# Optimization experiments

Hardware: AMD Instinct MI355X
Metric: run time of the kernel (lower is better)

The kernel has to match this reference:

```python
import jax, jax.numpy as jnp
import numpy as np

N_NODES = 50000
N_EDGES = 600000
IN_DIM = 64
HID = 128
LN_EPS = 1e-5


def setup_inputs() -> dict:
    key = jax.random.key(0)
    ks = jax.random.split(key, 10)
    x = jax.random.normal(ks[0], (N_NODES, IN_DIM), dtype=jnp.float32)
    edge_index = jax.random.randint(ks[1], (2, N_EDGES), 0, N_NODES, dtype=jnp.int64)
    def lin(k, fan_in, fan_out):
        bound = 1.0 / np.sqrt(fan_in)
        kw, kb = jax.random.split(k)
        W = jax.random.uniform(kw, (fan_in, fan_out), minval=-bound, maxval=bound, dtype=jnp.float32)
        b = jax.random.uniform(kb, (fan_out,), minval=-bound, maxval=bound, dtype=jnp.float32)
        return W, b
    W1, b1 = lin(ks[2], IN_DIM, HID)
    W2, b2 = lin(ks[3], HID, HID)
    W3, b3 = lin(ks[4], HID, HID)
    g1 = jnp.ones((HID,), jnp.float32); be1 = jnp.zeros((HID,), jnp.float32)
    g2 = jnp.ones((HID,), jnp.float32); be2 = jnp.zeros((HID,), jnp.float32)
    g3 = jnp.ones((HID,), jnp.float32); be3 = jnp.zeros((HID,), jnp.float32)
    return dict(x=x, edge_index=edge_index, W1=W1, b1=b1, W2=W2, b2=b2, W3=W3, b3=b3,
                g1=g1, be1=be1, g2=g2, be2=be2, g3=g3, be3=be3)


def _gnn_layer(h, W, b, src, dst, inv_cnt, g, be):
    # linear transform then mean aggregation over {neighbors ∪ self} (self-loops in src/dst)
    h = h @ W + b                                   # [N, HID]
    s = jax.ops.segment_sum(h[src], dst, num_segments=N_NODES)  # gather + scatter-sum
    h = s * inv_cnt                                 # mean aggregation
    h = jax.nn.relu(h)
    mu = jnp.mean(h, axis=-1, keepdims=True)
    var = jnp.var(h, axis=-1, keepdims=True)
    return g * (h - mu) * jax.lax.rsqrt(var + LN_EPS) + be


def reference(x, edge_index, W1, b1, W2, b2, W3, b3, g1, be1, g2, be2, g3, be3):
    loops = jnp.arange(N_NODES, dtype=edge_index.dtype)
    src = jnp.concatenate([edge_index[0], loops])   # message source (x_j)
    dst = jnp.concatenate([edge_index[1], loops])   # aggregation target
    cnt = jax.ops.segment_sum(jnp.ones_like(dst, dtype=x.dtype), dst, num_segments=N_NODES)
    inv_cnt = (1.0 / cnt)[:, None]                  # cnt >= 1 due to self loops
    h = _gnn_layer(x, W1, b1, src, dst, inv_cnt, g1, be1)
    h = _gnn_layer(h, W2, b2, src, dst, inv_cnt, g2, be2)
    h = _gnn_layer(h, W3, b3, src, dst, inv_cnt, g3, be3)
    return h
```

## Files before the change

kernel.cpp:

```cpp
#include <hip/hip_runtime.h>
#include <hip/hip_bf16.h>

#define N_NODES 50000
#define N_EDGES 600000
#define HID 128
#define LN_EPS 1e-5f

#define SCAN_BLOCK 1024
#define SCAN_NBLK ((N_NODES + SCAN_BLOCK - 1) / SCAN_BLOCK)

typedef __attribute__((ext_vector_type(8))) short bf16x8;
typedef __attribute__((ext_vector_type(4))) float f32x4;

static __device__ __forceinline__ unsigned short f2bf(float f) {
    union { float f; unsigned u; } v; v.f = f;
    unsigned u = v.u;
    u += 0x7fffu + ((u >> 16) & 1u);
    return (unsigned short)(u >> 16);
}
static __device__ __forceinline__ float bflo(unsigned u) {
    union { unsigned u; float f; } c; c.u = u << 16; return c.f;
}
static __device__ __forceinline__ float bfhi(unsigned u) {
    union { unsigned u; float f; } c; c.u = u & 0xffff0000u; return c.f;
}

__global__ __launch_bounds__(256) void count_kernel(const int* __restrict__ ei,
                                                    int* __restrict__ deg, int E) {
    int i = blockIdx.x * blockDim.x + threadIdx.x;
    if (i < E) atomicAdd(&deg[ei[E + i]], 1);
}

__global__ __launch_bounds__(SCAN_BLOCK) void deg_partial_kernel(const int* __restrict__ deg,
                                                                 int* __restrict__ partials, int n) {
    int t = threadIdx.x;
    int i = blockIdx.x * SCAN_BLOCK + t;
    int v = (i < n) ? deg[i] : 0;
    int s = v;
#pragma unroll
    for (int off = 1; off < 64; off <<= 1) s += __shfl_xor(s, off);
    __shared__ int ws[SCAN_BLOCK / 64];
    if ((t & 63) == 0) ws[t >> 6] = s;
    __syncthreads();
    if (t == 0) {
        int tot = 0;
#pragma unroll
        for (int w = 0; w < SCAN_BLOCK / 64; ++w) tot += ws[w];
        partials[blockIdx.x] = tot;
    }
}

__global__ __launch_bounds__(64) void scan_partials_kernel(int* __restrict__ partials,
                                                           int* __restrict__ row_ptr, int nblk) {
    int lane = threadIdx.x;
    int v = (lane < nblk) ? partials[lane] : 0;
    int incl = v;
#pragma unroll
    for (int off = 1; off < 64; off <<= 1) {
        int x = __shfl_up(incl, off);
        if (lane >= off) incl += x;
    }
    if (lane < nblk) partials[lane] = incl - v;
    if (lane == 63) row_ptr[N_NODES] = incl;
}

__global__ __launch_bounds__(SCAN_BLOCK) void scan_final_kernel(const int* __restrict__ deg,
                                                                const int* __restrict__ partials,
                                                                int* __restrict__ row_ptr,
                                                                int* __restrict__ cursor,
                                                                float* __restrict__ inv_cnt, int n) {
    int t = threadIdx.x;
    int i = blockIdx.x * SCAN_BLOCK + t;
    int v = (i < n) ? deg[i] : 0;
    int lane = t & 63, wid = t >> 6;
    int incl = v;
#pragma unroll
    for (int off = 1; off < 64; off <<= 1) {
        int x = __shfl_up(incl, off);
        if (lane >= off) incl += x;
    }
    __shared__ int ws[SCAN_BLOCK / 64];
    if (lane == 63) ws[wid] = incl;
    __syncthreads();
    int woff = 0;
    for (int w = 0; w < wid; ++w) woff += ws[w];
    int excl = partials[blockIdx.x] + woff + (incl - v);
    if (i < n) {
        row_ptr[i] = excl;
        cursor[i]  = excl;
        inv_cnt[i] = 1.0f / (float)(v + 1);
    }
}

__global__ __launch_bounds__(256) void fill_kernel(const int* __restrict__ ei,
                                                   int* __restrict__ cursor,
                                                   int* __restrict__ col, int E) {
    int i = blockIdx.x * blockDim.x + threadIdx.x;
    if (i < E) {
        int s = ei[i];
        int d = ei[E + i];
        int p = atomicAdd(&cursor[d], 1);
        col[p] = s;
    }
}

__global__ __launch_bounds__(256) void wswz_all_kernel(const float* __restrict__ W1,
                                                       const float* __restrict__ W2,
                                                       const float* __restrict__ W3,
                                                       unsigned short* __restrict__ d1,
                                                       unsigned short* __restrict__ d2,
                                                       unsigned short* __restrict__ d3) {
    int i = blockIdx.x * 256 + threadIdx.x;
    const float* W; unsigned short* dst; int idx;
    if (i < 64 * 128)              { W = W1; dst = d1; idx = i; }
    else if (i < (64 + 128) * 128) { W = W2; dst = d2; idx = i - 64 * 128; }
    else if (i < (64 + 256) * 128) { W = W3; dst = d3; idx = i - (64 + 128) * 128; }
    else return;
    int k = idx >> 7, col = idx & 127;
    dst[(((k >> 3) * 128) + col) * 8 + (k & 7)] = f2bf(W[idx]);
}

template <int K, int AF32>
__global__ __launch_bounds__(256) void gemm_mfma_kernel(
    const void* __restrict__ Ap,
    const unsigned short* __restrict__ Wswz,
    const float* __restrict__ bias,
    unsigned short* __restrict__ out, int N) {
    __shared__ unsigned short Bl[K * 128];
    __shared__ float bl[128];
    int t = threadIdx.x;
    for (int i = t; i < K * 16; i += 256)
        ((int4*)Bl)[i] = ((const int4*)Wswz)[i];
    if (t < 128) bl[t] = bias[t];
    __syncthreads();

    int lane = t & 63;
    int w = t >> 6;
    int r0 = blockIdx.x * 64 + w * 16;
    int colb = lane & 15;
    int kg = lane >> 4;
    int rowa = min(r0 + colb, N - 1);

    f32x4 acc[8];
#pragma unroll
    for (int c = 0; c < 8; ++c) acc[c] = (f32x4){0.f, 0.f, 0.f, 0.f};

    const bf16x8* Blv = (const bf16x8*)Bl;
    for (int s = 0; s < K; s += 32) {
        bf16x8 afrag;
        if (AF32) {
            const float* Af = (const float*)Ap;
            float4 a0 = *(const float4*)&Af[(size_t)rowa * K + s + kg * 8];
            float4 a1 = *(const float4*)&Af[(size_t)rowa * K + s + kg * 8 + 4];
            afrag[0] = (short)f2bf(a0.x); afrag[1] = (short)f2bf(a0.y);
            afrag[2] = (short)f2bf(a0.z); afrag[3] = (short)f2bf(a0.w);
            afrag[4] = (short)f2bf(a1.x); afrag[5] = (short)f2bf(a1.y);
            afrag[6] = (short)f2bf(a1.z); afrag[7] = (short)f2bf(a1.w);
        } else {
            const unsigned short* Ab = (const unsigned short*)Ap;
            afrag = *(const bf16x8*)&Ab[(size_t)rowa * K + s + kg * 8];
        }
        int kb = (s >> 3) + kg;
#pragma unroll
        for (int c = 0; c < 8; ++c) {
            bf16x8 bfrag = Blv[kb * 128 + c * 16 + colb];
            acc[c] = __builtin_amdgcn_mfma_f32_16x16x32_bf16(afrag, bfrag, acc[c], 0, 0, 0);
        }
    }
#pragma unroll
    for (int c = 0; c < 8; ++c) {
        int col = c * 16 + colb;
        float bv = bl[col];
#pragma unroll
        for (int r = 0; r < 4; ++r) {
            int ro = r0 + kg * 4 + r;
            if (ro < N) out[(size_t)ro * 128 + col] = f2bf(acc[c][r] + bv);
        }
    }
}

template <int BF16OUT>
__global__ __launch_bounds__(256) void agg_norm_kernel(
    const unsigned short* __restrict__ hb,
    const int* __restrict__ row_ptr,
    const int* __restrict__ col,
    const float* __restrict__ inv_cnt,
    const float* __restrict__ g, const float* __restrict__ be,
    void* __restrict__ outp, int N) {
    int tid  = blockIdx.x * 256 + threadIdx.x;
    int wave = tid >> 6;
    int lane = threadIdx.x & 63;
    int sub  = lane >> 4;
    int lc   = lane & 15;
    int n    = wave * 4 + sub;
    bool act = n < N;
    int nc   = act ? n : N - 1;

    const uint4* h4 = (const uint4*)hb;

    float a[8];
    {
        uint4 u = h4[(size_t)nc * 16 + lc];
        a[0] = bflo(u.x); a[1] = bfhi(u.x);
        a[2] = bflo(u.y); a[3] = bfhi(u.y);
        a[4] = bflo(u.z); a[5] = bfhi(u.z);
        a[6] = bflo(u.w); a[7] = bfhi(u.w);
    }

    int beg = row_ptr[nc], end = row_ptr[nc + 1];
    int cnt = end - beg;
    int lim = min(cnt, 32);
    int c0 = (lc < cnt)      ? col[beg + lc]      : nc;
    int c1 = (16 + lc < cnt) ? col[beg + 16 + lc] : nc;

    int wlim = lim;
    wlim = max(wlim, __shfl_xor(wlim, 16));
    wlim = max(wlim, __shfl_xor(wlim, 32));
    int nGrp = (wlim + 7) >> 3;

    for (int gi = 0; gi < nGrp; ++gi) {
        int e0 = gi * 8;
        int jj[8]; float mm[8];
#pragma unroll
        for (int q = 0; q < 8; ++q) {
            int iq = max(min(e0 + q, lim - 1), 0);
            mm[q] = (e0 + q < lim) ? 1.0f : 0.0f;
            int sl = sub * 16 + (iq & 15);
            int jA = __shfl(c0, sl);
            int jB = __shfl(c1, sl);
            jj[q] = (iq < 16) ? jA : jB;
        }
        uint4 u[8];
#pragma unroll
        for (int q = 0; q < 8; ++q) u[q] = h4[(size_t)jj[q] * 16 + lc];
#pragma unroll
        for (int q = 0; q < 8; ++q) {
            a[0] = fmaf(mm[q], bflo(u[q].x), a[0]); a[1] = fmaf(mm[q], bfhi(u[q].x), a[1]);
            a[2] = fmaf(mm[q], bflo(u[q].y), a[2]); a[3] = fmaf(mm[q], bfhi(u[q].y), a[3]);
            a[4] = fmaf(mm[q], bflo(u[q].z), a[4]); a[5] = fmaf(mm[q], bfhi(u[q].z), a[5]);
            a[6] = fmaf(mm[q], bflo(u[q].w), a[6]); a[7] = fmaf(mm[q], bfhi(u[q].w), a[7]);
        }
    }
    for (int e = 32; e < cnt; ++e) {
        int j = col[beg + e];
        uint4 u = h4[(size_t)j * 16 + lc];
        a[0] += bflo(u.x); a[1] += bfhi(u.x);
        a[2] += bflo(u.y); a[3] += bfhi(u.y);
        a[4] += bflo(u.z); a[5] += bfhi(u.z);
        a[6] += bflo(u.w); a[7] += bfhi(u.w);
    }

    float ic = inv_cnt[nc];
    float s[8], sum = 0.f, sq = 0.f;
#pragma unroll
    for (int k = 0; k < 8; ++k) {
        s[k] = fmaxf(a[k] * ic, 0.0f);
        sum += s[k];
        sq  += s[k] * s[k];
    }
#pragma unroll
    for (int off = 1; off < 16; off <<= 1) {
        sum += __shfl_xor(sum, off);
        sq  += __shfl_xor(sq, off);
    }
    float mu  = sum * (1.0f / 128.0f);
    float var = sq * (1.0f / 128.0f) - mu * mu;
    float rs  = rsqrtf(var + LN_EPS);

    const float4* gv  = (const float4*)g;
    const float4* bv  = (const float4*)be;
    float4 gA = gv[lc * 2], gB = gv[lc * 2 + 1];
    float4 bA = bv[lc * 2], bB = bv[lc * 2 + 1];
    float o[8];
    o[0] = gA.x * (s[0] - mu) * rs + bA.x;
    o[1] = gA.y * (s[1] - mu) * rs + bA.y;
    o[2] = gA.z * (s[2] - mu) * rs + bA.z;
    o[3] = gA.w * (s[3] - mu) * rs + bA.w;
    o[4] = gB.x * (s[4] - mu) * rs + bB.x;
    o[5] = gB.y * (s[5] - mu) * rs + bB.y;
    o[6] = gB.z * (s[6] - mu) * rs + bB.z;
    o[7] = gB.w * (s[7] - mu) * rs + bB.w;

    if (!act) return;
    if (BF16OUT) {
        uint4 p;
        p.x = (unsigned)f2bf(o[0]) | ((unsigned)f2bf(o[1]) << 16);
        p.y = (unsigned)f2bf(o[2]) | ((unsigned)f2bf(o[3]) << 16);
        p.z = (unsigned)f2bf(o[4]) | ((unsigned)f2bf(o[5]) << 16);
        p.w = (unsigned)f2bf(o[6]) | ((unsigned)f2bf(o[7]) << 16);
        ((uint4*)outp)[(size_t)nc * 16 + lc] = p;
    } else {
        float4 f0; f0.x = o[0]; f0.y = o[1]; f0.z = o[2]; f0.w = o[3];
        float4 f1; f1.x = o[4]; f1.y = o[5]; f1.z = o[6]; f1.w = o[7];
        ((float4*)outp)[(size_t)nc * 32 + lc * 2]     = f0;
        ((float4*)outp)[(size_t)nc * 32 + lc * 2 + 1] = f1;
    }
}

extern "C" void kernel_launch(void* const* d_in, const int* in_sizes, int n_in,
                              void* d_out, int out_size, void* d_ws, size_t ws_size,
                              hipStream_t stream) {
    const float* x  = (const float*)d_in[0];
    const int*   ei = (const int*)d_in[1];
    const float* W1 = (const float*)d_in[2];
    const float* b1 = (const float*)d_in[3];
    const float* W2 = (const float*)d_in[4];
    const float* b2 = (const float*)d_in[5];
    const float* W3 = (const float*)d_in[6];
    const float* b3 = (const float*)d_in[7];
    const float* g1 = (const float*)d_in[8];
    const float* be1 = (const float*)d_in[9];
    const float* g2 = (const float*)d_in[10];
    const float* be2 = (const float*)d_in[11];
    const float* g3 = (const float*)d_in[12];
    const float* be3 = (const float*)d_in[13];
    float* out = (float*)d_out;

    const int N = N_NODES, E = N_EDGES;
    char* w = (char*)d_ws;
    unsigned short* hb   = (unsigned short*)w; w += (size_t)N * 128 * 2;
    unsigned short* midb = (unsigned short*)w; w += (size_t)N * 128 * 2;
    unsigned short* w1s  = (unsigned short*)w; w += (size_t)64 * 128 * 2;
    unsigned short* w2s  = (unsigned short*)w; w += (size_t)128 * 128 * 2;
    unsigned short* w3s  = (unsigned short*)w; w += (size_t)128 * 128 * 2;
    int*   col    = (int*)w;    w += (size_t)E * sizeof(int);
    int*   rowp   = (int*)w;    w += (size_t)(N + 1) * sizeof(int);
    int*   cursor = (int*)w;    w += (size_t)N * sizeof(int);
    int*   deg    = (int*)w;    w += (size_t)N * sizeof(int);
    float* invc   = (float*)w;  w += (size_t)N * sizeof(float);
    int*   parts  = (int*)w;    w += (size_t)SCAN_NBLK * sizeof(int);

    hipMemsetAsync(deg, 0, (size_t)N * sizeof(int), stream);
    count_kernel<<<(E + 255) / 256, 256, 0, stream>>>(ei, deg, E);
    deg_partial_kernel<<<SCAN_NBLK, SCAN_BLOCK, 0, stream>>>(deg, parts, N);
    scan_partials_kernel<<<1, 64, 0, stream>>>(parts, rowp, SCAN_NBLK);
    scan_final_kernel<<<SCAN_NBLK, SCAN_BLOCK, 0, stream>>>(deg, parts, rowp, cursor, invc, N);
    fill_kernel<<<(E + 255) / 256, 256, 0, stream>>>(ei, cursor, col, E);

    wswz_all_kernel<<<((64 + 256) * 128 + 255) / 256, 256, 0, stream>>>(W1, W2, W3, w1s, w2s, w3s);

    const int gemm_blocks = (N + 63) / 64;
    const int agg_blocks  = (N + 15) / 16;

    gemm_mfma_kernel<64, 1><<<gemm_blocks, 256, 0, stream>>>(x, w1s, b1, hb, N);
    agg_norm_kernel<1><<<agg_blocks, 256, 0, stream>>>(hb, rowp, col, invc, g1, be1, midb, N);
    gemm_mfma_kernel<128, 0><<<gemm_blocks, 256, 0, stream>>>(midb, w2s, b2, hb, N);
    agg_norm_kernel<1><<<agg_blocks, 256, 0, stream>>>(hb, rowp, col, invc, g2, be2, midb, N);
    gemm_mfma_kernel<128, 0><<<gemm_blocks, 256, 0, stream>>>(midb, w3s, b3, hb, N);
    agg_norm_kernel<0><<<agg_blocks, 256, 0, stream>>>(hb, rowp, col, invc, g3, be3, out, N);
}
```

Measured before the change: 196.7 us.

## Fuse layer-1 GEMM, degree count, and weight swizzle into one launch; drop scan-partials kernel

Merges the first-layer GEMM (which now swizzles W1 into shared memory itself), the degree-counting atomics and the weight swizzle into one heterogeneous kernel whose blocks are split by block index. It also removes the single-block partials scan: each block of the final scan now sums the preceding partials serially in thread 0. The goal is fewer kernel launches and letting independent work run concurrently. In exchange, every GEMM block re-converts W1 and thread 0 does a serial loop over about 49 partials per block.

```diff
diff --git a/kernel.cpp b/kernel.cpp
--- a/kernel.cpp
+++ b/kernel.cpp
@@ -8,6 +8,10 @@
 
 #define SCAN_BLOCK 1024
 #define SCAN_NBLK ((N_NODES + SCAN_BLOCK - 1) / SCAN_BLOCK)
+
+#define GB1 ((N_NODES + 63) / 64)
+#define CB  ((N_EDGES + 255) / 256)
+#define WB  (((64 + 256) * 128) / 256)
 
 typedef __attribute__((ext_vector_type(8))) short bf16x8;
 typedef __attribute__((ext_vector_type(4))) float f32x4;
@@ -25,10 +29,82 @@
     union { unsigned u; float f; } c; c.u = u & 0xffff0000u; return c.f;
 }
 
-__global__ __launch_bounds__(256) void count_kernel(const int* __restrict__ ei,
-                                                    int* __restrict__ deg, int E) {
-    int i = blockIdx.x * blockDim.x + threadIdx.x;
-    if (i < E) atomicAdd(&deg[ei[E + i]], 1);
+__global__ __launch_bounds__(256) void mega1_kernel(
+    const float* __restrict__ x,
+    const unsigned short* __restrict__ W1swz,
+    const float* __restrict__ b1,
+    unsigned short* __restrict__ hb,
+    const int* __restrict__ ei,
+    int* __restrict__ deg,
+    const float* __restrict__ W1,
+    const float* __restrict__ W2,
+    const float* __restrict__ W3,
+    unsigned short* __restrict__ d1,
+    unsigned short* __restrict__ d2,
+    unsigned short* __restrict__ d3, int N, int E) {
+    __shared__ unsigned short Bl[64 * 128];
+    __shared__ float bl[128];
+    int bid = blockIdx.x;
+    int t = threadIdx.x;
+
+    if (bid < GB1) {
+        for (int i = t; i < 64 * 128; i += 256) {
+            int k = i >> 7, col = i & 127;
+            Bl[(((k >> 3) * 128) + col) * 8 + (k & 7)] = f2bf(W1[i]);
+        }
+        if (t < 128) bl[t] = b1[t];
+        __syncthreads();
+
+        int lane = t & 63;
+        int w = t >> 6;
+        int r0 = bid * 64 + w * 16;
+        int colb = lane & 15;
+        int kg = lane >> 4;
+        int rowa = min(r0 + colb, N - 1);
+
+        f32x4 acc[8];
+#pragma unroll
+        for (int c = 0; c < 8; ++c) acc[c] = (f32x4){0.f, 0.f, 0.f, 0.f};
+
+        const bf16x8* Blv = (const bf16x8*)Bl;
+        for (int s = 0; s < 64; s += 32) {
+            bf16x8 afrag;
+            float4 a0 = *(const float4*)&x[(size_t)rowa * 64 + s + kg * 8];
+            float4 a1 = *(const float4*)&x[(size_t)rowa * 64 + s + kg * 8 + 4];
+            afrag[0] = (short)f2bf(a0.x); afrag[1] = (short)f2bf(a0.y);
+            afrag[2] = (short)f2bf(a0.z); afrag[3] = (short)f2bf(a0.w);
+            afrag[4] = (short)f2bf(a1.x); afrag[5] = (short)f2bf(a1.y);
+            afrag[6] = (short)f2bf(a1.z); afrag[7] = (short)f2bf(a1.w);
+            int kb = (s >> 3) + kg;
+#pragma unroll
+            for (int c = 0; c < 8; ++c) {
+                bf16x8 bfrag = Blv[kb * 128 + c * 16 + colb];
+                acc[c] = __builtin_amdgcn_mfma_f32_16x16x32_bf16(afrag, bfrag, acc[c], 0, 0, 0);
+            }
+        }
+#pragma unroll
+        for (int c = 0; c < 8; ++c) {
+            int col = c * 16 + colb;
+            float bv = bl[col];
+#pragma unroll
+            for (int r = 0; r < 4; ++r) {
+                int ro = r0 + kg * 4 + r;
+                if (ro < N) hb[(size_t)ro * 128 + col] = f2bf(acc[c][r] + bv);
+            }
+        }
+    } else if (bid < GB1 + CB) {
+        int i = (bid - GB1) * 256 + t;
+        if (i < E) atomicAdd(&deg[ei[E + i]], 1);
+    } else {
+        int i = (bid - GB1 - CB) * 256 + t;
+        const float* W; unsigned short* dst; int idx;
+        if (i < 64 * 128)              { W = W1; dst = d1; idx = i; }
+        else if (i < (64 + 128) * 128) { W = W2; dst = d2; idx = i - 64 * 128; }
+        else if (i < (64 + 256) * 128) { W = W3; dst = d3; idx = i - (64 + 128) * 128; }
+        else return;
+        int k = idx >> 7, col = idx & 127;
+        dst[(((k >> 3) * 128) + col) * 8 + (k & 7)] = f2bf(W[idx]);
+    }
 }
 
 __global__ __launch_bounds__(SCAN_BLOCK) void deg_partial_kernel(const int* __restrict__ deg,
@@ -50,26 +126,24 @@
     }
 }
 
-__global__ __launch_bounds__(64) void scan_partials_kernel(int* __restrict__ partials,
-                                                           int* __restrict__ row_ptr, int nblk) {
-    int lane = threadIdx.x;
-    int v = (lane < nblk) ? partials[lane] : 0;
-    int incl = v;
-#pragma unroll
-    for (int off = 1; off < 64; off <<= 1) {
-        int x = __shfl_up(incl, off);
-        if (lane >= off) incl += x;
-    }
-    if (lane < nblk) partials[lane] = incl - v;
-    if (lane == 63) row_ptr[N_NODES] = incl;
-}
-
 __global__ __launch_bounds__(SCAN_BLOCK) void scan_final_kernel(const int* __restrict__ deg,
                                                                 const int* __restrict__ partials,
                                                                 int* __restrict__ row_ptr,
                                                                 int* __restrict__ cursor,
                                                                 float* __restrict__ inv_cnt, int n) {
+    __shared__ int base_sh;
+    __shared__ int ws[SCAN_BLOCK / 64];
     int t = threadIdx.x;
+    if (t == 0) {
+        int pre = 0, tot = 0;
+        for (int i = 0; i < SCAN_NBLK; ++i) {
+            int p = partials[i];
+            if (i < (int)blockIdx.x) pre += p;
+            tot += p;
+        }
+        base_sh = pre;
+        if (blockIdx.x == 0) row_ptr[n] = tot;
+    }
     int i = blockIdx.x * SCAN_BLOCK + t;
     int v = (i < n) ? deg[i] : 0;
     int lane = t & 63, wid = t >> 6;
@@ -79,12 +153,11 @@
         int x = __shfl_up(incl, off);
         if (lane >= off) incl += x;
     }
-    __shared__ int ws[SCAN_BLOCK / 64];
     if (lane == 63) ws[wid] = incl;
     __syncthreads();
     int woff = 0;
     for (int w = 0; w < wid; ++w) woff += ws[w];
-    int excl = partials[blockIdx.x] + woff + (incl - v);
+    int excl = base_sh + woff + (incl - v);
     if (i < n) {
         row_ptr[i] = excl;
         cursor[i]  = excl;
@@ -104,25 +177,9 @@
     }
 }
 
-__global__ __launch_bounds__(256) void wswz_all_kernel(const float* __restrict__ W1,
-                                                       const float* __restrict__ W2,
-                                                       const float* __restrict__ W3,
-                                                       unsigned short* __restrict__ d1,
-                                                       unsigned short* __restrict__ d2,
-                                                       unsigned short* __restrict__ d3) {
-    int i = blockIdx.x * 256 + threadIdx.x;
-    const float* W; unsigned short* dst; int idx;
-    if (i < 64 * 128)              { W = W1; dst = d1; idx = i; }
-    else if (i < (64 + 128) * 128) { W = W2; dst = d2; idx = i - 64 * 128; }
-    else if (i < (64 + 256) * 128) { W = W3; dst = d3; idx = i - (64 + 128) * 128; }
-    else return;
-    int k = idx >> 7, col = idx & 127;
-    dst[(((k >> 3) * 128) + col) * 8 + (k & 7)] = f2bf(W[idx]);
-}
-
-template <int K, int AF32>
+template <int K>
 __global__ __launch_bounds__(256) void gemm_mfma_kernel(
-    const void* __restrict__ Ap,
+    const unsigned short* __restrict__ Ab,
     const unsigned short* __restrict__ Wswz,
     const float* __restrict__ bias,
     unsigned short* __restrict__ out, int N) {
@@ -147,19 +204,7 @@
 
     const bf16x8* Blv = (const bf16x8*)Bl;
     for (int s = 0; s < K; s += 32) {
-        bf16x8 afrag;
-        if (AF32) {
-            const float* Af = (const float*)Ap;
-            float4 a0 = *(const float4*)&Af[(size_t)rowa * K + s + kg * 8];
-            float4 a1 = *(const float4*)&Af[(size_t)rowa * K + s + kg * 8 + 4];
-            afrag[0] = (short)f2bf(a0.x); afrag[1] = (short)f2bf(a0.y);
-            afrag[2] = (short)f2bf(a0.z); afrag[3] = (short)f2bf(a0.w);
-            afrag[4] = (short)f2bf(a1.x); afrag[5] = (short)f2bf(a1.y);
-            afrag[6] = (short)f2bf(a1.z); afrag[7] = (short)f2bf(a1.w);
-        } else {
-            const unsigned short* Ab = (const unsigned short*)Ap;
-            afrag = *(const bf16x8*)&Ab[(size_t)rowa * K + s + kg * 8];
-        }
+        bf16x8 afrag = *(const bf16x8*)&Ab[(size_t)rowa * K + s + kg * 8];
         int kb = (s >> 3) + kg;
 #pragma unroll
         for (int c = 0; c < 8; ++c) {
@@ -331,21 +376,19 @@
     int*   parts  = (int*)w;    w += (size_t)SCAN_NBLK * sizeof(int);
 
     hipMemsetAsync(deg, 0, (size_t)N * sizeof(int), stream);
-    count_kernel<<<(E + 255) / 256, 256, 0, stream>>>(ei, deg, E);
+
+    mega1_kernel<<<GB1 + CB + WB, 256, 0, stream>>>(x, w1s, b1, hb, ei, deg,
+                                                    W1, W2, W3, w1s, w2s, w3s, N, E);
     deg_partial_kernel<<<SCAN_NBLK, SCAN_BLOCK, 0, stream>>>(deg, parts, N);
-    scan_partials_kernel<<<1, 64, 0, stream>>>(parts, rowp, SCAN_NBLK);
     scan_final_kernel<<<SCAN_NBLK, SCAN_BLOCK, 0, stream>>>(deg, parts, rowp, cursor, invc, N);
     fill_kernel<<<(E + 255) / 256, 256, 0, stream>>>(ei, cursor, col, E);
 
-    wswz_all_kernel<<<((64 + 256) * 128 + 255) / 256, 256, 0, stream>>>(W1, W2, W3, w1s, w2s, w3s);
-
     const int gemm_blocks = (N + 63) / 64;
     const int agg_blocks  = (N + 15) / 16;
 
-    gemm_mfma_kernel<64, 1><<<gemm_blocks, 256, 0, stream>>>(x, w1s, b1, hb, N);
     agg_norm_kernel<1><<<agg_blocks, 256, 0, stream>>>(hb, rowp, col, invc, g1, be1, midb, N);
-    gemm_mfma_kernel<128, 0><<<gemm_blocks, 256, 0, stream>>>(midb, w2s, b2, hb, N);
+    gemm_mfma_kernel<128><<<gemm_blocks, 256, 0, stream>>>(midb, w2s, b2, hb, N);
     agg_norm_kernel<1><<<agg_blocks, 256, 0, stream>>>(hb, rowp, col, invc, g2, be2, midb, N);
-    gemm_mfma_kernel<128, 0><<<gemm_blocks, 256, 0, stream>>>(midb, w3s, b3, hb, N);
+    gemm_mfma_kernel<128><<<gemm_blocks, 256, 0, stream>>>(midb, w3s, b3, hb, N);
     agg_norm_kernel<0><<<agg_blocks, 256, 0, stream>>>(hb, rowp, col, invc, g3, be3, out, N);
 }
```

Result: faster. 185.4 us (-5.7%).
